# Kernel optimization log

Hardware: AMD Instinct MI355X
Metric: run time of the kernel (lower is better)

Reference implementation:

```python
import jax, jax.numpy as jnp
import numpy as np

B = 131072
IN, H1, H2, OUT = 784, 128, 64, 10


def setup_inputs() -> dict:
    key = jax.random.key(0)
    ks = jax.random.split(key, 10)
    f16 = jnp.float16
    x = jax.random.normal(ks[0], (B, IN), dtype=f16)
    # int4 quantized weights: values in [-8, 7], stored as int32
    w1_q = jax.random.randint(ks[1], (H1, IN), -8, 8, dtype=jnp.int32)
    w2_q = jax.random.randint(ks[2], (H2, H1), -8, 8, dtype=jnp.int32)
    w3_q = jax.random.randint(ks[3], (OUT, H2), -8, 8, dtype=jnp.int32)
    # per-output-channel scales ~ kaiming-ish magnitude / 7 (int4 max)
    s1 = (jax.random.uniform(ks[4], (H1,), dtype=f16) * f16(0.02) + f16(0.005))
    s2 = (jax.random.uniform(ks[5], (H2,), dtype=f16) * f16(0.02) + f16(0.005))
    s3 = (jax.random.uniform(ks[6], (OUT,), dtype=f16) * f16(0.02) + f16(0.005))
    b1 = jax.random.normal(ks[7], (H1,), dtype=f16) * f16(0.01)
    b2 = jax.random.normal(ks[8], (H2,), dtype=f16) * f16(0.01)
    b3 = jax.random.normal(ks[9], (OUT,), dtype=f16) * f16(0.01)
    return {"x": x, "w1_q": w1_q, "s1": s1, "b1": b1,
            "w2_q": w2_q, "s2": s2, "b2": b2,
            "w3_q": w3_q, "s3": s3, "b3": b3}


def _qlinear(x, w_q, scale, bias):
    # W4A16: dequantize int4 weights with per-out-channel scale, fp16 GEMM + bias
    w = w_q.astype(jnp.float16) * scale[:, None]  # [out, in]
    return jnp.dot(x, w.T) + bias


def reference(x, w1_q, s1, b1, w2_q, s2, b2, w3_q, s3, b3):
    x = x.reshape(-1, IN)
    h = jax.nn.relu(_qlinear(x, w1_q, s1, b1))
    h = jax.nn.relu(_qlinear(h, w2_q, s2, b2))
    return _qlinear(h, w3_q, s3, b3)
```

## Files before the change

### kernel.cpp

```cpp
#include <hip/hip_runtime.h>
#include <hip/hip_bf16.h>

#define NROWS 131072
#define KIN   784
#define H1N   128
#define H2N   64
#define OUTN  10

#define W1C_ELEMS (100 * 128 * 8)
#define W2C_ELEMS (16 * 64 * 8)
#define W3_ELEMS  (16 * 64)

typedef short s16x8 __attribute__((ext_vector_type(8)));
typedef float f32x4 __attribute__((ext_vector_type(4)));

typedef __hip_bfloat16 bf16;

static __device__ __forceinline__ short b2s(float f) {
    bf16 h = __float2bfloat16(f);
    return *reinterpret_cast<short*>(&h);
}

static __device__ __forceinline__ s16x8 cvt8(f32x4 a, f32x4 b) {
    s16x8 r;
    r[0] = b2s(a[0]); r[1] = b2s(a[1]); r[2] = b2s(a[2]); r[3] = b2s(a[3]);
    r[4] = b2s(b[0]); r[5] = b2s(b[1]); r[6] = b2s(b[2]); r[7] = b2s(b[3]);
    return r;
}

static __device__ __forceinline__ void gl2lds16(const void* g, char* l) {
    __builtin_amdgcn_global_load_lds(
        (const __attribute__((address_space(1))) void*)g,
        (__attribute__((address_space(3))) void*)l, 16, 0, 0);
}

#define WAITV(N) do { asm volatile("s_waitcnt vmcnt(" #N ")" ::: "memory"); \
                      __builtin_amdgcn_sched_barrier(0); } while (0)
#define WAITL()  do { asm volatile("s_waitcnt lgkmcnt(0)" ::: "memory"); \
                      __builtin_amdgcn_sched_barrier(0); } while (0)
#define BAR()    __builtin_amdgcn_s_barrier()

__global__ __launch_bounds__(256) void dequant_kernel(
    const int* __restrict__ w1q, const float* __restrict__ s1,
    const int* __restrict__ w2q, const float* __restrict__ s2,
    const int* __restrict__ w3q, const float* __restrict__ s3,
    bf16* __restrict__ w1c, bf16* __restrict__ w2c, bf16* __restrict__ w3d)
{
    const int total = W1C_ELEMS + W2C_ELEMS + W3_ELEMS;
    for (int i = blockIdx.x * blockDim.x + threadIdx.x; i < total;
         i += gridDim.x * blockDim.x) {
        if (i < W1C_ELEMS) {
            int kb = i >> 10, rem = i & 1023;
            int col = rem >> 3, j = rem & 7;
            int k = kb * 8 + j;
            float v = 0.0f;
            if (k < KIN) v = (float)w1q[col * KIN + k] * s1[col];
            w1c[i] = __float2bfloat16(v);
        } else if (i < W1C_ELEMS + W2C_ELEMS) {
            int t = i - W1C_ELEMS;
            int kb = t >> 9, rem = t & 511;
            int col = rem >> 3, j = rem & 7;
            int k = kb * 8 + j;
            w2c[t] = __float2bfloat16((float)w2q[col * H1N + k] * s2[col]);
        } else {
            int t = i - W1C_ELEMS - W2C_ELEMS;
            int r = t >> 6, c = t & 63;
            float v = 0.0f;
            if (r < OUTN) v = (float)w3q[r * H2N + c] * s3[r];
            w3d[t] = __float2bfloat16(v);
        }
    }
}

__global__ __launch_bounds__(256, 5) void mlp_kernel(
    const float* __restrict__ x,
    const bf16*  __restrict__ w1c,
    const bf16*  __restrict__ w2c,
    const bf16*  __restrict__ w3d,
    const float* __restrict__ b1,
    const float* __restrict__ b2,
    const float* __restrict__ b3,
    float* __restrict__ out)
{
    __shared__ __align__(16) char lds[32768];

    const int tid  = threadIdx.x;
    const int lane = tid & 63;
    const int wv   = tid >> 6;
    const int r16  = lane & 15;
    const int kg   = lane >> 4;
    const int kgo  = kg * 8;

    const int i3 = lane >> 3;
    const int i7 = lane & 7;
    const int sw = i7 ^ (i3 & 7);

    const long long rowW = (long long)blockIdx.x * 64 + wv * 16;
    const float* gA0 = x + (rowW + i3) * (long long)KIN + sw * 4;
    const float* gA1 = x + (rowW + 8 + i3) * (long long)KIN + sw * 4;
    const bf16*  gB  = w1c + (size_t)wv * 1024 + (size_t)lane * 8;

    const int aoff0 = wv * 2048 + r16 * 128 + (((2 * kg)     ^ (r16 & 7)) * 16);
    const int aoff1 = wv * 2048 + r16 * 128 + (((2 * kg + 1) ^ (r16 & 7)) * 16);
    const int boff  = 8192 + kg * 2048 + r16 * 16;

#pragma unroll
    for (int w = 0; w < 2; ++w) {
        char* sd = lds + w * 16384;
        gl2lds16(gA0 + w * 32, sd + wv * 2048);
        gl2lds16(gA1 + w * 32, sd + wv * 2048 + 1024);
        const bf16* gw = gB + (size_t)w * 4096;
        gl2lds16(gw,       sd + 8192 + wv * 2048);
        gl2lds16(gw + 512, sd + 8192 + wv * 2048 + 1024);
    }

    f32x4 acc1[8];
#pragma unroll
    for (int j = 0; j < 8; ++j) acc1[j] = (f32x4){0.f, 0.f, 0.f, 0.f};

#pragma unroll 1
    for (int t = 0; t < 24; ++t) {
        WAITV(4);
        BAR();
        const char* sb = lds + (t & 1) * 16384;
        f32x4 q0 = *(const f32x4*)(sb + aoff0);
        f32x4 q1 = *(const f32x4*)(sb + aoff1);
        s16x8 bw[8];
#pragma unroll
        for (int nj = 0; nj < 8; ++nj)
            bw[nj] = *(const s16x8*)(sb + boff + nj * 256);
        WAITL();
        BAR();
        char* sd = lds + (t & 1) * 16384;
        const int w = t + 2;
        if (w < 24) {
            gl2lds16(gA0 + w * 32, sd + wv * 2048);
            gl2lds16(gA1 + w * 32, sd + wv * 2048 + 1024);
            const bf16* gw = gB + (size_t)w * 4096;
            gl2lds16(gw,       sd + 8192 + wv * 2048);
            gl2lds16(gw + 512, sd + 8192 + wv * 2048 + 1024);
        } else if (w == 24) {
            const int adj = (sw >= 4) ? 16 : 0;
            gl2lds16(gA0 + 768 - adj, sd + wv * 2048);
            gl2lds16(gA1 + 768 - adj, sd + wv * 2048 + 1024);
            const bf16* gw = gB + (size_t)24 * 4096;
            gl2lds16(gw,       sd + 8192 + wv * 2048);
            gl2lds16(gw + 512, sd + 8192 + wv * 2048 + 1024);
        }
        s16x8 a = cvt8(q0, q1);
#pragma unroll
        for (int nj = 0; nj < 8; ++nj)
            acc1[nj] = __builtin_amdgcn_mfma_f32_16x16x32_bf16(a, bw[nj], acc1[nj], 0, 0, 0);
    }
    {
        WAITV(0);
        BAR();
        const char* sb = lds;
        f32x4 q0 = *(const f32x4*)(sb + aoff0);
        f32x4 q1 = *(const f32x4*)(sb + aoff1);
        s16x8 bw[8];
#pragma unroll
        for (int nj = 0; nj < 8; ++nj)
            bw[nj] = *(const s16x8*)(sb + boff + nj * 256);
        WAITL();
        BAR();
        s16x8 a = cvt8(q0, q1);
#pragma unroll
        for (int nj = 0; nj < 8; ++nj)
            acc1[nj] = __builtin_amdgcn_mfma_f32_16x16x32_bf16(a, bw[nj], acc1[nj], 0, 0, 0);
    }

    char* ar = lds + wv * 4224;
    short (*h1w)[132] = (short(*)[132])ar;
#pragma unroll
    for (int nj = 0; nj < 8; ++nj) {
        const int col = nj * 16 + r16;
        const float bb = b1[col];
#pragma unroll
        for (int r = 0; r < 4; ++r)
            h1w[kg * 4 + r][col] = b2s(fmaxf(acc1[nj][r] + bb, 0.0f));
    }

    f32x4 acc2[4];
#pragma unroll
    for (int j = 0; j < 4; ++j) acc2[j] = (f32x4){0.f, 0.f, 0.f, 0.f};

#pragma unroll
    for (int it = 0; it < 4; ++it) {
        const int kk = it * 32 + kgo;
        s16x8 a = *(const s16x8*)&h1w[r16][kk];
        const bf16* bp2 = w2c + (size_t)(it * 4 + kg) * 512 + (size_t)r16 * 8;
#pragma unroll
        for (int nj = 0; nj < 4; ++nj) {
            s16x8 b = *(const s16x8*)(bp2 + nj * 128);
            acc2[nj] = __builtin_amdgcn_mfma_f32_16x16x32_bf16(a, b, acc2[nj], 0, 0, 0);
        }
    }

    short (*h2w)[68] = (short(*)[68])ar;
#pragma unroll
    for (int nj = 0; nj < 4; ++nj) {
        const int col = nj * 16 + r16;
        const float bb = b2[col];
#pragma unroll
        for (int r = 0; r < 4; ++r)
            h2w[kg * 4 + r][col] = b2s(fmaxf(acc2[nj][r] + bb, 0.0f));
    }

    f32x4 acc3 = (f32x4){0.f, 0.f, 0.f, 0.f};
#pragma unroll
    for (int it = 0; it < 2; ++it) {
        const int kk = it * 32 + kgo;
        s16x8 a = *(const s16x8*)&h2w[r16][kk];
        s16x8 b = *(const s16x8*)(w3d + r16 * H2N + kk);
        acc3 = __builtin_amdgcn_mfma_f32_16x16x32_bf16(a, b, acc3, 0, 0, 0);
    }

    float* ob = (float*)ar;
    const float bb3 = (r16 < OUTN) ? b3[r16] : 0.0f;
#pragma unroll
    for (int r = 0; r < 4; ++r) {
        const int row = kg * 4 + r;
        if (r16 < OUTN) ob[row * OUTN + r16] = acc3[r] + bb3;
    }
    const long long obase = rowW * OUTN;
    for (int i = lane; i < 16 * OUTN; i += 64) out[obase + i] = ob[i];
}

extern "C" void kernel_launch(void* const* d_in, const int* in_sizes, int n_in,
                              void* d_out, int out_size, void* d_ws, size_t ws_size,
                              hipStream_t stream) {
    const float* x   = (const float*)d_in[0];
    const int*   w1q = (const int*)d_in[1];
    const float* s1  = (const float*)d_in[2];
    const float* b1  = (const float*)d_in[3];
    const int*   w2q = (const int*)d_in[4];
    const float* s2  = (const float*)d_in[5];
    const float* b2  = (const float*)d_in[6];
    const int*   w3q = (const int*)d_in[7];
    const float* s3  = (const float*)d_in[8];
    const float* b3  = (const float*)d_in[9];
    float* out = (float*)d_out;

    bf16* w1c = (bf16*)d_ws;
    bf16* w2c = w1c + W1C_ELEMS;
    bf16* w3d = w2c + W2C_ELEMS;

    dequant_kernel<<<128, 256, 0, stream>>>(w1q, s1, w2q, s2, w3q, s3, w1c, w2c, w3d);
    mlp_kernel<<<NROWS / 64, 256, 0, stream>>>(x, w1c, w2c, w3d, b1, b2, b3, out);
}
```

Measured before the change: 112.0 us.

## Double block to 512 threads sharing W1 tile loads and stream x non-temporally

Each block now covers 128 rows with 8 waves instead of 64 rows with 4. Every wave loads only its share of the W1 tile, so the staged weights are reused across twice as many rows and per-row weight traffic into LDS is halved. Activation loads use the non-temporal cache hint so the streamed x does not evict cached weights. LDS grows to 48KB per block and occupancy bounds change, which can reduce the number of resident blocks per CU.

```diff
diff --git a/kernel.cpp b/kernel.cpp
--- a/kernel.cpp
+++ b/kernel.cpp
@@ -32,6 +32,11 @@
     __builtin_amdgcn_global_load_lds(
         (const __attribute__((address_space(1))) void*)g,
         (__attribute__((address_space(3))) void*)l, 16, 0, 0);
+}
+static __device__ __forceinline__ void gl2lds16_nt(const void* g, char* l) {
+    __builtin_amdgcn_global_load_lds(
+        (const __attribute__((address_space(1))) void*)g,
+        (__attribute__((address_space(3))) void*)l, 16, 0, 2);
 }
 
 #define WAITV(N) do { asm volatile("s_waitcnt vmcnt(" #N ")" ::: "memory"); \
@@ -72,7 +77,7 @@
     }
 }
 
-__global__ __launch_bounds__(256, 5) void mlp_kernel(
+__global__ __launch_bounds__(512, 6) void mlp_kernel(
     const float* __restrict__ x,
     const bf16*  __restrict__ w1c,
     const bf16*  __restrict__ w2c,
@@ -82,7 +87,7 @@
     const float* __restrict__ b3,
     float* __restrict__ out)
 {
-    __shared__ __align__(16) char lds[32768];
+    __shared__ __align__(16) char lds[49152];
 
     const int tid  = threadIdx.x;
     const int lane = tid & 63;
@@ -93,25 +98,23 @@
 
     const int i3 = lane >> 3;
     const int i7 = lane & 7;
-    const int sw = i7 ^ (i3 & 7);
-
-    const long long rowW = (long long)blockIdx.x * 64 + wv * 16;
-    const float* gA0 = x + (rowW + i3) * (long long)KIN + sw * 4;
-    const float* gA1 = x + (rowW + 8 + i3) * (long long)KIN + sw * 4;
-    const bf16*  gB  = w1c + (size_t)wv * 1024 + (size_t)lane * 8;
-
-    const int aoff0 = wv * 2048 + r16 * 128 + (((2 * kg)     ^ (r16 & 7)) * 16);
-    const int aoff1 = wv * 2048 + r16 * 128 + (((2 * kg + 1) ^ (r16 & 7)) * 16);
-    const int boff  = 8192 + kg * 2048 + r16 * 16;
+    const int sw = i7 ^ i3;
+    const int adj = (sw >= 4) ? 16 : 0;
+
+    const long long rowW = (long long)blockIdx.x * 128 + wv * 16;
+    const float* gA  = x + (rowW + i3) * (long long)KIN + sw * 4;
+    const bf16*  gBw = w1c + (size_t)wv * 512 + (size_t)lane * 8;
+
+    const int aoff0 = wv * 2048 + r16 * 128 + (((2 * kg) ^ (r16 & 7)) * 16);
+    const int boffc = 32768 + kg * 2048 + r16 * 16;
 
 #pragma unroll
     for (int w = 0; w < 2; ++w) {
-        char* sd = lds + w * 16384;
-        gl2lds16(gA0 + w * 32, sd + wv * 2048);
-        gl2lds16(gA1 + w * 32, sd + wv * 2048 + 1024);
-        const bf16* gw = gB + (size_t)w * 4096;
-        gl2lds16(gw,       sd + 8192 + wv * 2048);
-        gl2lds16(gw + 512, sd + 8192 + wv * 2048 + 1024);
+        char* ad = lds + w * 16384 + wv * 2048;
+        const float* g = gA + w * 32;
+        gl2lds16_nt(g, ad);
+        gl2lds16_nt(g + 8 * KIN, ad + 1024);
+        gl2lds16(gBw + (size_t)w * 4096, lds + 32768 + w * 8192 + wv * 1024);
     }
 
     f32x4 acc1[8];
@@ -120,32 +123,31 @@
 
 #pragma unroll 1
     for (int t = 0; t < 24; ++t) {
-        WAITV(4);
-        BAR();
-        const char* sb = lds + (t & 1) * 16384;
-        f32x4 q0 = *(const f32x4*)(sb + aoff0);
-        f32x4 q1 = *(const f32x4*)(sb + aoff1);
+        WAITV(3);
+        BAR();
+        const char* sa = lds + (t & 1) * 16384;
+        f32x4 q0 = *(const f32x4*)(sa + aoff0);
+        f32x4 q1 = *(const f32x4*)(sa + (aoff0 ^ 16));
+        const char* sb = lds + (t & 1) * 8192 + boffc;
         s16x8 bw[8];
 #pragma unroll
-        for (int nj = 0; nj < 8; ++nj)
-            bw[nj] = *(const s16x8*)(sb + boff + nj * 256);
+        for (int nj = 0; nj < 8; ++nj) bw[nj] = *(const s16x8*)(sb + nj * 256);
         WAITL();
         BAR();
-        char* sd = lds + (t & 1) * 16384;
-        const int w = t + 2;
-        if (w < 24) {
-            gl2lds16(gA0 + w * 32, sd + wv * 2048);
-            gl2lds16(gA1 + w * 32, sd + wv * 2048 + 1024);
-            const bf16* gw = gB + (size_t)w * 4096;
-            gl2lds16(gw,       sd + 8192 + wv * 2048);
-            gl2lds16(gw + 512, sd + 8192 + wv * 2048 + 1024);
-        } else if (w == 24) {
-            const int adj = (sw >= 4) ? 16 : 0;
-            gl2lds16(gA0 + 768 - adj, sd + wv * 2048);
-            gl2lds16(gA1 + 768 - adj, sd + wv * 2048 + 1024);
-            const bf16* gw = gB + (size_t)24 * 4096;
-            gl2lds16(gw,       sd + 8192 + wv * 2048);
-            gl2lds16(gw + 512, sd + 8192 + wv * 2048 + 1024);
+        if (t < 22) {
+            char* ad = lds + (t & 1) * 16384 + wv * 2048;
+            const float* g = gA + (t + 2) * 32;
+            gl2lds16_nt(g, ad);
+            gl2lds16_nt(g + 8 * KIN, ad + 1024);
+            gl2lds16(gBw + (size_t)(t + 2) * 4096,
+                     lds + 32768 + (t & 1) * 8192 + wv * 1024);
+        } else if (t == 22) {
+            char* ad = lds + (t & 1) * 16384 + wv * 2048;
+            const float* g = gA + 768 - adj;
+            gl2lds16_nt(g, ad);
+            gl2lds16_nt(g + 8 * KIN, ad + 1024);
+            gl2lds16(gBw + (size_t)24 * 4096,
+                     lds + 32768 + (t & 1) * 8192 + wv * 1024);
         }
         s16x8 a = cvt8(q0, q1);
 #pragma unroll
@@ -155,13 +157,13 @@
     {
         WAITV(0);
         BAR();
-        const char* sb = lds;
-        f32x4 q0 = *(const f32x4*)(sb + aoff0);
-        f32x4 q1 = *(const f32x4*)(sb + aoff1);
+        const char* sa = lds;
+        f32x4 q0 = *(const f32x4*)(sa + aoff0);
+        f32x4 q1 = *(const f32x4*)(sa + (aoff0 ^ 16));
+        const char* sb = lds + boffc;
         s16x8 bw[8];
 #pragma unroll
-        for (int nj = 0; nj < 8; ++nj)
-            bw[nj] = *(const s16x8*)(sb + boff + nj * 256);
+        for (int nj = 0; nj < 8; ++nj) bw[nj] = *(const s16x8*)(sb + nj * 256);
         WAITL();
         BAR();
         s16x8 a = cvt8(q0, q1);
@@ -247,5 +249,5 @@
     bf16* w3d = w2c + W2C_ELEMS;
 
     dequant_kernel<<<128, 256, 0, stream>>>(w1q, s1, w2q, s2, w3q, s3, w1c, w2c, w3d);
-    mlp_kernel<<<NROWS / 64, 256, 0, stream>>>(x, w1c, w2c, w3d, b1, b2, b3, out);
-}
+    mlp_kernel<<<NROWS / 128, 512, 0, stream>>>(x, w1c, w2c, w3d, b1, b2, b3, out);
+}
```

Measured after the change: 211.0 us. 1.88x slower.
